# Kernel tuning notes

Hardware: AMD Instinct MI355X
Metric: run time of the kernel (lower is better)

The kernel has to match this reference:

```python
import jax, jax.numpy as jnp
import numpy as np

MARGIN = 2.0

def setup_inputs() -> dict:
    key = jax.random.key(0)
    k1, k2 = jax.random.split(key)
    n = 8192
    preds = jax.random.normal(k1, (n,), dtype=jnp.float32)
    labels = jax.random.normal(k2, (n,), dtype=jnp.float32)
    return {"preds": preds, "labels": labels}

def reference(preds, labels):
    # sum over pairs (i, j) with j > i of relu(-(p_j - p_i) * sign(l_j - l_i) + margin)
    n = preds.shape[0]
    pd = preds[None, :] - preds[:, None]          # [n, n], entry (i, j) = p_j - p_i
    ls = jnp.sign(labels[None, :] - labels[:, None])  # [n, n], sign(l_j - l_i)
    hinge = jax.nn.relu(-pd * ls + MARGIN)        # [n, n]
    mask = jnp.triu(jnp.ones((n, n), dtype=hinge.dtype), k=1)  # j > i only
    return jnp.sum(hinge * mask)
```

## Files before the change

### kernel.cpp

```cpp
#include <hip/hip_runtime.h>

#define MARGIN 2.0f
#define TILE 256
#define NT 32
#define NBLK (NT * (NT + 1) / 2)

__global__ __launch_bounds__(TILE) void BatchRankingLoss_kernel(
    const float* __restrict__ preds, const float* __restrict__ labels,
    float* __restrict__ partials)
{
    const int bid = blockIdx.x;
    int r = (int)((sqrtf(8.0f * (float)bid + 1.0f) - 1.0f) * 0.5f);
    while ((r + 1) * (r + 2) / 2 <= bid) ++r;
    while (r * (r + 1) / 2 > bid) --r;
    const int c = bid - r * (r + 1) / 2;
    const int ti = c, tj = r;

    const int tid = threadIdx.x;

    __shared__ __align__(16) float2 sj[TILE];
    const int jg = tj * TILE + tid;
    sj[tid] = make_float2(preds[jg], labels[jg]);
    __syncthreads();

    const int ig = ti * TILE + tid;
    const float pi = preds[ig];
    const float li = labels[ig];

    float sum = 0.0f;
    if (ti == tj) {
        #pragma unroll 4
        for (int j = 0; j < TILE; ++j) {
            const float2 v = sj[j];
            const float d  = pi - v.x;
            const float s  = __builtin_copysignf(1.0f, v.y - li);
            const float t  = fmaxf(fmaf(d, s, MARGIN), 0.0f);
            sum += (j > tid) ? t : 0.0f;
        }
    } else {
        #pragma unroll 8
        for (int j = 0; j < TILE; ++j) {
            const float2 v = sj[j];
            const float d  = pi - v.x;
            const float s  = __builtin_copysignf(1.0f, v.y - li);
            sum += fmaxf(fmaf(d, s, MARGIN), 0.0f);
        }
    }

    #pragma unroll
    for (int off = 32; off > 0; off >>= 1)
        sum += __shfl_down(sum, off, 64);

    __shared__ float wsum[TILE / 64];
    const int lane = tid & 63, wid = tid >> 6;
    if (lane == 0) wsum[wid] = sum;
    __syncthreads();

    if (tid == 0) {
        float b = wsum[0] + wsum[1] + wsum[2] + wsum[3];
        partials[bid] = b;
    }
}

__global__ __launch_bounds__(256) void BatchRankingLoss_reduce(
    const float* __restrict__ partials, float* __restrict__ out)
{
    const int tid = threadIdx.x;
    float s = 0.0f;
    for (int k = tid; k < NBLK; k += 256) s += partials[k];
    #pragma unroll
    for (int off = 32; off > 0; off >>= 1)
        s += __shfl_down(s, off, 64);
    __shared__ float wsum[4];
    const int lane = tid & 63, wid = tid >> 6;
    if (lane == 0) wsum[wid] = s;
    __syncthreads();
    if (tid == 0) out[0] = wsum[0] + wsum[1] + wsum[2] + wsum[3];
}

extern "C" void kernel_launch(void* const* d_in, const int* in_sizes, int n_in,
                              void* d_out, int out_size, void* d_ws, size_t ws_size,
                              hipStream_t stream) {
    const float* preds  = (const float*)d_in[0];
    const float* labels = (const float*)d_in[1];
    float* out = (float*)d_out;
    float* partials = (float*)d_ws;

    BatchRankingLoss_kernel<<<NBLK, TILE, 0, stream>>>(preds, labels, partials);
    BatchRankingLoss_reduce<<<1, 256, 0, stream>>>(partials, out);
}
```

Measured before the change: 64.32 us.

## Split tile pairs into half-column blocks, dual accumulators, atomic final reduction

Each triangular tile pair is now handled by two blocks, each covering half of the j columns, which doubles the grid to about 1056 blocks for better CU occupancy. The inner loop uses two independent accumulators to shorten the FP add dependency chain. The separate reduce kernel is replaced by a per-block atomicAdd into the output, with a tiny zeroing kernel launched first. The cost is that float atomics make the summation order nondeterministic, and each block's i-side loads are now repeated across the two halves.

```diff
diff --git a/kernel.cpp b/kernel.cpp
--- a/kernel.cpp
+++ b/kernel.cpp
@@ -2,51 +2,82 @@
 
 #define MARGIN 2.0f
 #define TILE 256
+#define HALF 128
 #define NT 32
-#define NBLK (NT * (NT + 1) / 2)
+#define NPAIR (NT * (NT + 1) / 2)
+#define NBLK (NPAIR * 2)
+
+__global__ __launch_bounds__(64) void BatchRankingLoss_zero(float* __restrict__ out)
+{
+    if (threadIdx.x == 0) out[0] = 0.0f;
+}
 
 __global__ __launch_bounds__(TILE) void BatchRankingLoss_kernel(
     const float* __restrict__ preds, const float* __restrict__ labels,
-    float* __restrict__ partials)
+    float* __restrict__ out)
 {
-    const int bid = blockIdx.x;
-    int r = (int)((sqrtf(8.0f * (float)bid + 1.0f) - 1.0f) * 0.5f);
-    while ((r + 1) * (r + 2) / 2 <= bid) ++r;
-    while (r * (r + 1) / 2 > bid) --r;
-    const int c = bid - r * (r + 1) / 2;
+    const int bid  = blockIdx.x;
+    const int pair = bid >> 1;
+    const int half = bid & 1;
+
+    int r = (int)((sqrtf(8.0f * (float)pair + 1.0f) - 1.0f) * 0.5f);
+    while ((r + 1) * (r + 2) / 2 <= pair) ++r;
+    while (r * (r + 1) / 2 > pair) --r;
+    const int c  = pair - r * (r + 1) / 2;
     const int ti = c, tj = r;
 
     const int tid = threadIdx.x;
+    const int j0  = half * HALF;
 
-    __shared__ __align__(16) float2 sj[TILE];
-    const int jg = tj * TILE + tid;
-    sj[tid] = make_float2(preds[jg], labels[jg]);
+    __shared__ __align__(16) float2 sj[HALF];
+    if (tid < HALF) {
+        const int jg = tj * TILE + j0 + tid;
+        sj[tid] = make_float2(preds[jg], labels[jg]);
+    }
     __syncthreads();
 
-    const int ig = ti * TILE + tid;
+    const int   ig = ti * TILE + tid;
     const float pi = preds[ig];
     const float li = labels[ig];
 
-    float sum = 0.0f;
+    float s0 = 0.0f, s1 = 0.0f;
     if (ti == tj) {
-        #pragma unroll 4
-        for (int j = 0; j < TILE; ++j) {
-            const float2 v = sj[j];
-            const float d  = pi - v.x;
-            const float s  = __builtin_copysignf(1.0f, v.y - li);
-            const float t  = fmaxf(fmaf(d, s, MARGIN), 0.0f);
-            sum += (j > tid) ? t : 0.0f;
+        #pragma unroll 8
+        for (int j = 0; j < HALF; j += 2) {
+            {
+                const float2 v = sj[j];
+                const float  t = fmaxf(fmaf(pi - v.x,
+                                            __builtin_copysignf(1.0f, v.y - li),
+                                            MARGIN), 0.0f);
+                s0 += (j0 + j > tid) ? t : 0.0f;
+            }
+            {
+                const float2 v = sj[j + 1];
+                const float  t = fmaxf(fmaf(pi - v.x,
+                                            __builtin_copysignf(1.0f, v.y - li),
+                                            MARGIN), 0.0f);
+                s1 += (j0 + j + 1 > tid) ? t : 0.0f;
+            }
         }
     } else {
-        #pragma unroll 8
-        for (int j = 0; j < TILE; ++j) {
-            const float2 v = sj[j];
-            const float d  = pi - v.x;
-            const float s  = __builtin_copysignf(1.0f, v.y - li);
-            sum += fmaxf(fmaf(d, s, MARGIN), 0.0f);
+        #pragma unroll 16
+        for (int j = 0; j < HALF; j += 2) {
+            {
+                const float2 v = sj[j];
+                s0 += fmaxf(fmaf(pi - v.x,
+                                 __builtin_copysignf(1.0f, v.y - li),
+                                 MARGIN), 0.0f);
+            }
+            {
+                const float2 v = sj[j + 1];
+                s1 += fmaxf(fmaf(pi - v.x,
+                                 __builtin_copysignf(1.0f, v.y - li),
+                                 MARGIN), 0.0f);
+            }
         }
     }
 
+    float sum = s0 + s1;
     #pragma unroll
     for (int off = 32; off > 0; off >>= 1)
         sum += __shfl_down(sum, off, 64);
@@ -56,26 +87,8 @@
     if (lane == 0) wsum[wid] = sum;
     __syncthreads();
 
-    if (tid == 0) {
-        float b = wsum[0] + wsum[1] + wsum[2] + wsum[3];
-        partials[bid] = b;
-    }
-}
-
-__global__ __launch_bounds__(256) void BatchRankingLoss_reduce(
-    const float* __restrict__ partials, float* __restrict__ out)
-{
-    const int tid = threadIdx.x;
-    float s = 0.0f;
-    for (int k = tid; k < NBLK; k += 256) s += partials[k];
-    #pragma unroll
-    for (int off = 32; off > 0; off >>= 1)
-        s += __shfl_down(s, off, 64);
-    __shared__ float wsum[4];
-    const int lane = tid & 63, wid = tid >> 6;
-    if (lane == 0) wsum[wid] = s;
-    __syncthreads();
-    if (tid == 0) out[0] = wsum[0] + wsum[1] + wsum[2] + wsum[3];
+    if (tid == 0)
+        atomicAdd(out, wsum[0] + wsum[1] + wsum[2] + wsum[3]);
 }
 
 extern "C" void kernel_launch(void* const* d_in, const int* in_sizes, int n_in,
@@ -84,8 +97,7 @@
     const float* preds  = (const float*)d_in[0];
     const float* labels = (const float*)d_in[1];
     float* out = (float*)d_out;
-    float* partials = (float*)d_ws;
 
-    BatchRankingLoss_kernel<<<NBLK, TILE, 0, stream>>>(preds, labels, partials);
-    BatchRankingLoss_reduce<<<1, 256, 0, stream>>>(partials, out);
+    BatchRankingLoss_zero<<<1, 64, 0, stream>>>(out);
+    BatchRankingLoss_kernel<<<NBLK, TILE, 0, stream>>>(preds, labels, out);
 }
```

Result: slower. 73.07 us (+13.6%).
